# Performance work log

Measured on AMD Instinct MI355X. Metric: run time of the kernel, lower is better.

## Reference

```python
import jax, jax.numpy as jnp
import numpy as np

NEG_SLOPE = 0.2  # PyG GATConv leaky_relu negative_slope
EPS = 1e-16      # PyG softmax denominator epsilon


def _add_self_loops(edge_index, edge_attr, N):
    # PyG add_self_loops with fill_value='mean': loop attr = mean of incoming edge attrs
    src, dst = edge_index[0], edge_index[1]
    ones = jnp.ones((src.shape[0],), edge_attr.dtype)
    cnt = jax.ops.segment_sum(ones, dst, num_segments=N)
    loop_attr = jax.ops.segment_sum(edge_attr, dst, num_segments=N) / jnp.maximum(cnt, 1.0)[:, None]
    loops = jnp.arange(N, dtype=src.dtype)
    return (jnp.concatenate([src, loops]),
            jnp.concatenate([dst, loops]),
            jnp.concatenate([edge_attr, loop_attr], axis=0))


def _gat_conv(x, src, dst, ea, W, We, att_src, att_dst, att_edge, bias, heads, out_ch):
    N = x.shape[0]
    h = (x @ W).reshape(N, heads, out_ch)              # [N,H,C]
    a_src = (h * att_src).sum(-1)                      # [N,H]
    a_dst = (h * att_dst).sum(-1)                      # [N,H]
    e = (ea @ We).reshape(-1, heads, out_ch)           # [E,H,C]
    a_edge = (e * att_edge).sum(-1)                    # [E,H]
    alpha = jax.nn.leaky_relu(a_src[src] + a_dst[dst] + a_edge, NEG_SLOPE)
    amax = jax.ops.segment_max(alpha, dst, num_segments=N)
    alpha = jnp.exp(alpha - amax[dst])
    denom = jax.ops.segment_sum(alpha, dst, num_segments=N)
    alpha = alpha / (denom[dst] + EPS)
    out = jax.ops.segment_sum(h[src] * alpha[..., None], dst, num_segments=N)  # [N,H,C]
    return out.mean(axis=1) + bias                     # concat=False -> mean over heads


def setup_inputs() -> dict:
    key = jax.random.key(0)
    ks = jax.random.split(key, 16)
    N, E, F_in, HID, OUT, H = 50000, 800000, 64, 16, 8, 8
    s = 0.1
    return {
        "x": jax.random.normal(ks[0], (N, F_in), jnp.float32),
        "edge_index": jax.random.randint(ks[1], (2, E), 0, N, dtype=jnp.int64),
        "edge_attr": jax.random.uniform(ks[2], (E, 1), jnp.float32),
        "W1": jax.random.normal(ks[3], (F_in, H * HID), jnp.float32) * s,
        "We1": jax.random.normal(ks[4], (1, H * HID), jnp.float32) * s,
        "att_src1": jax.random.normal(ks[5], (H, HID), jnp.float32) * s,
        "att_dst1": jax.random.normal(ks[6], (H, HID), jnp.float32) * s,
        "att_edge1": jax.random.normal(ks[7], (H, HID), jnp.float32) * s,
        "b1": jnp.zeros((HID,), jnp.float32),
        "W2": jax.random.normal(ks[8], (HID, OUT), jnp.float32) * s,
        "We2": jax.random.normal(ks[9], (1, OUT), jnp.float32) * s,
        "att_src2": jax.random.normal(ks[10], (1, OUT), jnp.float32) * s,
        "att_dst2": jax.random.normal(ks[11], (1, OUT), jnp.float32) * s,
        "att_edge2": jax.random.normal(ks[12], (1, OUT), jnp.float32) * s,
        "b2": jnp.zeros((OUT,), jnp.float32),
    }


def reference(x, edge_index, edge_attr, W1, We1, att_src1, att_dst1, att_edge1, b1,
              W2, We2, att_src2, att_dst2, att_edge2, b2):
    N = x.shape[0]
    src, dst, ea = _add_self_loops(edge_index, edge_attr, N)
    h = jax.nn.relu(_gat_conv(x, src, dst, ea, W1, We1, att_src1, att_dst1, att_edge1, b1, 8, 16))
    # dropout is identity in eval mode
    return _gat_conv(h, src, dst, ea, W2, We2, att_src2, att_dst2, att_edge2, b2, 1, 8)
```

## Files before the change

kernel.cpp:

```cpp
#include <hip/hip_runtime.h>
#include <hip/hip_fp16.h>
#include <math.h>

#define LRELU(x) ((x) > 0.0f ? (x) : 0.2f * (x))
#define EPS 1e-16f

typedef _Float16 half8 __attribute__((ext_vector_type(8)));
typedef float floatx4 __attribute__((ext_vector_type(4)));

#define RNG 4
#define NRR 16384
#define RB  64


__global__ __launch_bounds__(256) void k_hist(int E, int CH, const int* __restrict__ ei,
                                              int* __restrict__ H, int* __restrict__ rank) {
    int r = blockIdx.x / RB, b = blockIdx.x % RB;
    __shared__ int hist[NRR];
    for (int i = threadIdx.x; i < NRR; i += 256) hist[i] = 0;
    __syncthreads();
    int lo = b * CH, hi = min(E, (b + 1) * CH);
    int rlo = r << 14;
#pragma unroll 4
    for (int e = lo + threadIdx.x; e < hi; e += 256) {
        int d = ei[E + e];
        int dr = d - rlo;
        if ((unsigned)dr < NRR) rank[e] = atomicAdd(&hist[dr], 1);
    }
    __syncthreads();
    int* Hb = H + (size_t)blockIdx.x * NRR;
    for (int i = threadIdx.x; i < NRR; i += 256) Hb[i] = hist[i];
}

__global__ __launch_bounds__(256) void k_cntscan(int N, int* __restrict__ H,
                                                 int* rowptr, int* bsums) {
    __shared__ int sm[256];
    int t = threadIdx.x;
    int n = blockIdx.x * 256 + t;
    int sum = 0;
    if (n < N) {
        int r = n >> 14, dr = n & (NRR - 1);
        size_t base = ((size_t)(r * RB)) * NRR + dr;
#pragma unroll 8
        for (int b = 0; b < RB; ++b) {
            size_t idx = base + (size_t)b * NRR;
            int v = H[idx];
            H[idx] = sum;
            sum += v;
        }
    }
    int val = (n < N) ? (sum + 1) : 0;
    sm[t] = val; __syncthreads();
    for (int ofs = 1; ofs < 256; ofs <<= 1) {
        int v = (t >= ofs) ? sm[t - ofs] : 0;
        __syncthreads();
        sm[t] += v;
        __syncthreads();
    }
    if (n < N) rowptr[n] = sm[t] - val;
    if (t == 255) bsums[blockIdx.x] = sm[255];
}

__global__ void k_scan2(int nb, int N, int* bsums, int* rowptr) {
    __shared__ int sm[256];
    int t = threadIdx.x;
    int v = (t < nb) ? bsums[t] : 0;
    sm[t] = v; __syncthreads();
    for (int ofs = 1; ofs < 256; ofs <<= 1) {
        int u = (t >= ofs) ? sm[t - ofs] : 0;
        __syncthreads();
        sm[t] += u;
        __syncthreads();
    }
    if (t < nb) bsums[t] = sm[t] - v;
    if (t == 255) rowptr[N] = sm[255];
}

__global__ void k_scan3(int N, int* rowptr, const int* __restrict__ bsums) {
    int n = blockIdx.x * blockDim.x + threadIdx.x;
    if (n < N) rowptr[n] += bsums[n >> 8];
}

__global__ void k_scatter(int E, int CH, const int* __restrict__ ei, const float* __restrict__ ea,
                          const int* __restrict__ rowptr, const int* __restrict__ H,
                          const int* __restrict__ rank, int2* __restrict__ rec) {
    int e = blockIdx.x * blockDim.x + threadIdx.x;
    if (e >= E) return;
    int s = ei[e], d = ei[E + e];
    int r = d >> 14, dr = d & (NRR - 1);
    int b = e / CH;
    int pos = rowptr[d] + H[((size_t)(r * RB + b)) * NRR + dr] + rank[e];
    unsigned long long pk = ((unsigned long long)(unsigned)__float_as_int(ea[e]) << 32)
                          | (unsigned long long)(unsigned)s;
    __builtin_nontemporal_store(pk, (unsigned long long*)&rec[pos]);
}


__global__ __launch_bounds__(256) void k_misc(
    int N, int nbN, int Mpad, const int* __restrict__ rowptr, int2* __restrict__ rec,
    const float* __restrict__ x, _Float16* __restrict__ xh,
    const float* __restrict__ W1, _Float16* __restrict__ Wpk,
    const float* __restrict__ We1, const float* __restrict__ ae1,
    const float* __restrict__ We2, const float* __restrict__ ae2,
    float* __restrict__ wed) {
    int bid = blockIdx.x;
    if (bid < nbN) {
        int d = bid * 256 + threadIdx.x;
        if (d < N) {
            int start = rowptr[d], slot = rowptr[d + 1] - 1;
            float ssum = 0.0f;
            for (int i = start; i < slot; ++i) ssum += __int_as_float(rec[i].y);
            float mean = ssum / fmaxf((float)(slot - start), 1.0f);
            rec[slot] = make_int2(d, __float_as_int(mean));
        }
    } else if (bid < nbN + Mpad / 32) {
        int t = (bid - nbN) * 256 + threadIdx.x;
        int row = t >> 3;
        half8 h;
        if (row < N) {
            const float4* pp = (const float4*)(x + (size_t)t * 8);
            float4 f0 = pp[0], f1 = pp[1];
            h[0] = (_Float16)f0.x; h[1] = (_Float16)f0.y; h[2] = (_Float16)f0.z; h[3] = (_Float16)f0.w;
            h[4] = (_Float16)f1.x; h[5] = (_Float16)f1.y; h[6] = (_Float16)f1.z; h[7] = (_Float16)f1.w;
        } else {
#pragma unroll
            for (int i = 0; i < 8; ++i) h[i] = (_Float16)0.0f;
        }
        *(half8*)(xh + (size_t)t * 8) = h;
    } else {
        int t = threadIdx.x;
        for (int i = 0; i < 32; ++i) {
            int idx = i * 256 + t;
            int j  = idx & 7;
            int lq = (idx >> 3) & 63;
            int ks = (idx >> 9) & 1;
            int ct = idx >> 10;
            int k   = ks * 32 + (lq >> 4) * 8 + j;
            int col = ct * 16 + (lq & 15);
            Wpk[idx] = (_Float16)W1[k * 128 + col];
        }
        if (t < 8) {
            float ssum = 0.0f;
            for (int cc = 0; cc < 16; ++cc) ssum += We1[t * 16 + cc] * ae1[t * 16 + cc];
            wed[t] = ssum;
        }
        if (t == 8) {
            float ssum = 0.0f;
            for (int cc = 0; cc < 8; ++cc) ssum += We2[cc] * ae2[cc];
            wed[8] = ssum;
        }
    }
}


#define LDSP 132

__global__ __launch_bounds__(256) void k_gemm1m(
    int N, const _Float16* __restrict__ xh, const _Float16* __restrict__ Wpk,
    const float* __restrict__ att_s, const float* __restrict__ att_d,
    __half* __restrict__ h1, float* __restrict__ asrc, float* __restrict__ adst) {
    __shared__ float hs[4 * 16 * LDSP];
    int tid = threadIdx.x;
    int w = tid >> 6, l = tid & 63;
    int row0 = blockIdx.x * 64 + w * 16;
    int arow = row0 + (l & 15);
    half8 a0 = *(const half8*)(xh + (size_t)arow * 64 + (l >> 4) * 8);
    half8 a1 = *(const half8*)(xh + (size_t)arow * 64 + 32 + (l >> 4) * 8);
    float* base = &hs[w * 16 * LDSP];
    int r0 = (l >> 4) * 4;
#pragma unroll
    for (int ct = 0; ct < 8; ++ct) {
        half8 b0 = *(const half8*)(Wpk + ((ct * 2 + 0) * 64 + l) * 8);
        half8 b1 = *(const half8*)(Wpk + ((ct * 2 + 1) * 64 + l) * 8);
        floatx4 acc = {0.f, 0.f, 0.f, 0.f};
        acc = __builtin_amdgcn_mfma_f32_16x16x32_f16(a0, b0, acc, 0, 0, 0);
        acc = __builtin_amdgcn_mfma_f32_16x16x32_f16(a1, b1, acc, 0, 0, 0);
        int col = ct * 16 + (l & 15);
#pragma unroll
        for (int i = 0; i < 4; ++i)
            base[(r0 + i) * LDSP + col] = acc[i];
    }
    __syncthreads();
    int r = tid >> 2, g = tid & 3;
    int rg = blockIdx.x * 64 + r;
    if (rg >= N) return;
    float v[32];
    const float* rp = &hs[r * LDSP + g * 32];
#pragma unroll
    for (int j = 0; j < 8; ++j) {
        floatx4 t4 = *(const floatx4*)(rp + j * 4);
        v[j * 4 + 0] = t4[0]; v[j * 4 + 1] = t4[1];
        v[j * 4 + 2] = t4[2]; v[j * 4 + 3] = t4[3];
    }
    float vs0 = 0.f, vs1 = 0.f, vd0 = 0.f, vd1 = 0.f;
    const float4* as4 = (const float4*)(att_s + g * 32);
    const float4* ad4 = (const float4*)(att_d + g * 32);
#pragma unroll
    for (int j = 0; j < 4; ++j) {
        float4 a4 = as4[j], d4 = ad4[j];
        vs0 += v[j*4+0]*a4.x + v[j*4+1]*a4.y + v[j*4+2]*a4.z + v[j*4+3]*a4.w;
        vd0 += v[j*4+0]*d4.x + v[j*4+1]*d4.y + v[j*4+2]*d4.z + v[j*4+3]*d4.w;
    }
#pragma unroll
    for (int j = 4; j < 8; ++j) {
        float4 a4 = as4[j], d4 = ad4[j];
        vs1 += v[j*4+0]*a4.x + v[j*4+1]*a4.y + v[j*4+2]*a4.z + v[j*4+3]*a4.w;
        vd1 += v[j*4+0]*d4.x + v[j*4+1]*d4.y + v[j*4+2]*d4.z + v[j*4+3]*d4.w;
    }
    union { __half h[32]; float4 f4[4]; } u;
#pragma unroll
    for (int i = 0; i < 32; ++i) u.h[i] = __float2half(v[i]);
    float4* hp = (float4*)(h1 + (size_t)rg * 128 + g * 32);
#pragma unroll
    for (int j = 0; j < 4; ++j) hp[j] = u.f4[j];
    asrc[rg * 8 + g * 2]     = vs0;
    asrc[rg * 8 + g * 2 + 1] = vs1;
    adst[rg * 8 + g * 2]     = vd0;
    adst[rg * 8 + g * 2 + 1] = vd1;
}


__global__ __launch_bounds__(256) void k_agg1(
    int N, const int* __restrict__ rowptr, const int2* __restrict__ rec,
    const float* __restrict__ asrc1, const float* __restrict__ adst1,
    const float* __restrict__ wed,
    const __half* __restrict__ h1, const float* __restrict__ b1,
    const float* __restrict__ W2, const float* __restrict__ as2w, const float* __restrict__ ad2w,
    float* __restrict__ hh2, float* __restrict__ asrc2, float* __restrict__ adst2) {
    int wid = (blockIdx.x * blockDim.x + threadIdx.x) >> 6;
    if (wid >= N) return;
    int l = threadIdx.x & 63;
    int g = l >> 4, q = l & 15, hq = q >> 1;
    int start = rowptr[wid], end = rowptr[wid + 1];
    int len = end - start;
    int G = (len + 3) >> 2;
    int nIt = (G + 1) >> 1;
    int startB = start + (nIt << 2);
    int endA = min(startB, end);
    float adn = adst1[wid * 8 + hq];
    float wdh = wed[hq];

    float acc[8] = {0.f,0.f,0.f,0.f,0.f,0.f,0.f,0.f};
    float denom = 0.0f;
    int eA = start + g, eB = startB + g;
    int last = end - 1;
    int2 rvA = rec[min(eA, last)];
    int2 rvB = rec[min(eB, last)];
    float avA = asrc1[rvA.x * 8 + hq];
    float avB = asrc1[rvB.x * 8 + hq];
    for (int it = 0; it < nIt; ++it) {
        float4 hvA = *(const float4*)(h1 + ((size_t)rvA.x << 7) + q * 8);
        float4 hvB = *(const float4*)(h1 + ((size_t)rvB.x << 7) + q * 8);
        int eAn = eA + 4, eBn = eB + 4;
        int2 rnA = rec[min(eAn, last)];
        int2 rnB = rec[min(eBn, last)];
        float anA = asrc1[rnA.x * 8 + hq];
        float anB = asrc1[rnB.x * 8 + hq];
        float aA = avA + adn + __int_as_float(rvA.y) * wdh;
        aA = LRELU(aA);
        float pA = (eA < endA) ? __expf(aA) : 0.0f;
        float aB = avB + adn + __int_as_float(rvB.y) * wdh;
        aB = LRELU(aB);
        float pB = (eB < end) ? __expf(aB) : 0.0f;
        denom += pA + pB;
        const _Float16* hpA = (const _Float16*)&hvA;
        const _Float16* hpB = (const _Float16*)&hvB;
#pragma unroll
        for (int k = 0; k < 8; ++k)
            acc[k] = fmaf(pA, (float)hpA[k], fmaf(pB, (float)hpB[k], acc[k]));
        rvA = rnA; avA = anA; rvB = rnB; avB = anB;
        eA = eAn; eB = eBn;
    }
#pragma unroll
    for (int k = 0; k < 8; ++k) {
        acc[k] += __shfl_xor(acc[k], 16);
        acc[k] += __shfl_xor(acc[k], 32);
    }
    denom += __shfl_xor(denom, 16);
    denom += __shfl_xor(denom, 32);
    float inv = 1.0f / (denom + EPS);
    float val[8];
#pragma unroll
    for (int k = 0; k < 8; ++k) {
        float v = acc[k] * inv;
        v += __shfl_xor(v, 2);
        v += __shfl_xor(v, 4);
        v += __shfl_xor(v, 8);
        val[k] = v;
    }
    int par = l & 1;
    int c = (l >> 1) & 7;
    float t8[8];
#pragma unroll
    for (int j = 0; j < 8; ++j)
        t8[j] = fmaxf(val[j] * 0.125f + b1[par * 8 + j], 0.0f);
    float partial = 0.0f;
#pragma unroll
    for (int j = 0; j < 8; ++j)
        partial = fmaf(t8[j], W2[(par * 8 + j) * 8 + c], partial);
    float hhc = partial + __shfl_xor(partial, 1);
    float sdot = hhc * as2w[c];
    float ddot = hhc * ad2w[c];
    sdot += __shfl_xor(sdot, 2); sdot += __shfl_xor(sdot, 4); sdot += __shfl_xor(sdot, 8);
    ddot += __shfl_xor(ddot, 2); ddot += __shfl_xor(ddot, 4); ddot += __shfl_xor(ddot, 8);
    if (l < 16 && par == 0) hh2[(size_t)wid * 8 + c] = hhc;
    if (l == 0) { asrc2[wid] = sdot; adst2[wid] = ddot; }
}


__global__ __launch_bounds__(256) void k_agg2(
    int N, const int* __restrict__ rowptr, const int2* __restrict__ rec,
    const float* __restrict__ asrc2, const float* __restrict__ adst2,
    const float* __restrict__ wed,
    const float* __restrict__ hh, const float* __restrict__ b2, float* __restrict__ out) {
    int wid = (blockIdx.x * blockDim.x + threadIdx.x) >> 6;
    if (wid >= N) return;
    int l = threadIdx.x & 63;
    int eo = l >> 3, c = l & 7;
    int start = rowptr[wid], end = rowptr[wid + 1];
    int len = end - start;
    int G = (len + 7) >> 3;
    int nIt = (G + 1) >> 1;
    int startB = start + (nIt << 3);
    int endA = min(startB, end);
    float adn = adst2[wid];
    float w2 = wed[8];

    float acc = 0.0f, denom = 0.0f;
    int eA = start + eo, eB = startB + eo;
    int last = end - 1;
    int2 rvA = rec[min(eA, last)];
    int2 rvB = rec[min(eB, last)];
    float avA = asrc2[rvA.x];
    float avB = asrc2[rvB.x];
    for (int it = 0; it < nIt; ++it) {
        float hvA = hh[(size_t)rvA.x * 8 + c];
        float hvB = hh[(size_t)rvB.x * 8 + c];
        int eAn = eA + 8, eBn = eB + 8;
        int2 rnA = rec[min(eAn, last)];
        int2 rnB = rec[min(eBn, last)];
        float anA = asrc2[rnA.x];
        float anB = asrc2[rnB.x];
        float aA = avA + adn + __int_as_float(rvA.y) * w2;
        aA = LRELU(aA);
        float pA = (eA < endA) ? __expf(aA) : 0.0f;
        float aB = avB + adn + __int_as_float(rvB.y) * w2;
        aB = LRELU(aB);
        float pB = (eB < end) ? __expf(aB) : 0.0f;
        denom += pA + pB;
        acc = fmaf(pA, hvA, fmaf(pB, hvB, acc));
        rvA = rnA; avA = anA; rvB = rnB; avB = anB;
        eA = eAn; eB = eBn;
    }
    acc += __shfl_xor(acc, 8);  acc += __shfl_xor(acc, 16);  acc += __shfl_xor(acc, 32);
    denom += __shfl_xor(denom, 8); denom += __shfl_xor(denom, 16); denom += __shfl_xor(denom, 32);
    if (l < 8) out[(size_t)wid * 8 + l] = acc / (denom + EPS) + b2[l];
}


extern "C" void kernel_launch(void* const* d_in, const int* in_sizes, int n_in,
                              void* d_out, int out_size, void* d_ws, size_t ws_size,
                              hipStream_t stream) {
    const float* x        = (const float*)d_in[0];
    const int*   ei       = (const int*)d_in[1];
    const float* ea       = (const float*)d_in[2];
    const float* W1       = (const float*)d_in[3];
    const float* We1      = (const float*)d_in[4];
    const float* att_src1 = (const float*)d_in[5];
    const float* att_dst1 = (const float*)d_in[6];
    const float* att_edge1= (const float*)d_in[7];
    const float* b1       = (const float*)d_in[8];
    const float* W2       = (const float*)d_in[9];
    const float* We2      = (const float*)d_in[10];
    const float* att_src2 = (const float*)d_in[11];
    const float* att_dst2 = (const float*)d_in[12];
    const float* att_edge2= (const float*)d_in[13];
    const float* b2       = (const float*)d_in[14];
    float* out = (float*)d_out;

    const int N = in_sizes[0] / 64;
    const int E = in_sizes[2];
    const int E2 = E + N;
    const int CH = (E + RB - 1) / RB;
    const int NB64 = (N + 63) / 64;
    const int Mpad = NB64 * 64;

    char* p = (char*)d_ws;
    auto alloc = [&](size_t bytes) { void* r = (void*)p; p += (bytes + 255) & ~(size_t)255; return r; };
    int*   rowptr = (int*)  alloc((size_t)(N + 1) * 4);
    int*   bsums  = (int*)  alloc((size_t)4096 * 4);
    int2*  rec    = (int2*) alloc((size_t)E2 * 8);
    _Float16* Wpk = (_Float16*)alloc((size_t)8192 * 2);
    __half* h1    = (__half*)alloc((size_t)Mpad * 128 * 2);
    float* asrc1  = (float*)alloc((size_t)N * 8 * 4);
    float* adst1  = (float*)alloc((size_t)N * 8 * 4);
    float* hh2    = (float*)alloc((size_t)N * 8 * 4);
    float* asrc2  = (float*)alloc((size_t)N * 4);
    float* adst2  = (float*)alloc((size_t)N * 4);
    float* wed    = (float*)alloc(16 * 4);
    char* pS = p;
    int*   rank  = (int*)pS;
    int*   H     = (int*)(pS + (((size_t)E * 4 + 255) & ~(size_t)255));
    _Float16* xh = (_Float16*)pS;

    const int nbN = (N + 255) / 256;

    hipLaunchKernelGGL(k_hist,    dim3(RNG * RB), dim3(256), 0, stream, E, CH, ei, H, rank);
    hipLaunchKernelGGL(k_cntscan, dim3(nbN), dim3(256), 0, stream, N, H, rowptr, bsums);
    hipLaunchKernelGGL(k_scan2,   dim3(1), dim3(256), 0, stream, nbN, N, bsums, rowptr);
    hipLaunchKernelGGL(k_scan3,   dim3(nbN), dim3(256), 0, stream, N, rowptr, bsums);
    hipLaunchKernelGGL(k_scatter, dim3((E + 255) / 256), dim3(256), 0, stream, E, CH, ei, ea, rowptr, H, rank, rec);
    hipLaunchKernelGGL(k_misc,    dim3(nbN + Mpad / 32 + 1), dim3(256), 0, stream, N, nbN, Mpad, rowptr,
                       rec, x, xh, W1, Wpk, We1, att_edge1, We2, att_edge2, wed);
    hipLaunchKernelGGL(k_gemm1m,  dim3(NB64), dim3(256), 0, stream, N, xh, Wpk, att_src1, att_dst1, h1, asrc1, adst1);
    hipLaunchKernelGGL(k_agg1,    dim3((N + 3) / 4), dim3(256), 0, stream, N, rowptr, rec, asrc1, adst1, wed,
                       h1, b1, W2, att_src2, att_dst2, hh2, asrc2, adst2);
    hipLaunchKernelGGL(k_agg2,    dim3((N + 3) / 4), dim3(256), 0, stream, N, rowptr, rec, asrc2, adst2, wed,
                       hh2, b2, out);
}
```

Before: 151.1 us.

## Remap layer-1 aggregation lanes to edge-by-head and prescale logits by log2e

In the layer-1 aggregation, each lane now takes one edge-slot and one head, loading 16 halfs per edge. Previously lanes split each 128-wide row into quarters across 4 edge groups, with two interleaved edge streams. The head-mean and W2 projection now go through an LDS transpose instead of shuffle chains. Attention logits are prescaled by log2(e) at production so the kernels use exp2f and a fmaxf-based leaky relu. Both aggregation kernels add a two-deep prefetch of edge records, which adds register pressure and LDS use.

```diff
diff --git a/kernel.cpp b/kernel.cpp
--- a/kernel.cpp
+++ b/kernel.cpp
@@ -2,8 +2,8 @@
 #include <hip/hip_fp16.h>
 #include <math.h>
 
-#define LRELU(x) ((x) > 0.0f ? (x) : 0.2f * (x))
 #define EPS 1e-16f
+#define LOG2E 1.44269504088896340736f
 
 typedef _Float16 half8 __attribute__((ext_vector_type(8)));
 typedef float floatx4 __attribute__((ext_vector_type(4)));
@@ -142,12 +142,12 @@
         if (t < 8) {
             float ssum = 0.0f;
             for (int cc = 0; cc < 16; ++cc) ssum += We1[t * 16 + cc] * ae1[t * 16 + cc];
-            wed[t] = ssum;
+            wed[t] = ssum * LOG2E;
         }
         if (t == 8) {
             float ssum = 0.0f;
             for (int cc = 0; cc < 8; ++cc) ssum += We2[cc] * ae2[cc];
-            wed[8] = ssum;
+            wed[8] = ssum * LOG2E;
         }
     }
 }
@@ -213,10 +213,10 @@
     float4* hp = (float4*)(h1 + (size_t)rg * 128 + g * 32);
 #pragma unroll
     for (int j = 0; j < 4; ++j) hp[j] = u.f4[j];
-    asrc[rg * 8 + g * 2]     = vs0;
-    asrc[rg * 8 + g * 2 + 1] = vs1;
-    adst[rg * 8 + g * 2]     = vd0;
-    adst[rg * 8 + g * 2 + 1] = vd1;
+    asrc[rg * 8 + g * 2]     = vs0 * LOG2E;
+    asrc[rg * 8 + g * 2 + 1] = vs1 * LOG2E;
+    adst[rg * 8 + g * 2]     = vd0 * LOG2E;
+    adst[rg * 8 + g * 2 + 1] = vd1 * LOG2E;
 }
 
 
@@ -224,87 +224,77 @@
     int N, const int* __restrict__ rowptr, const int2* __restrict__ rec,
     const float* __restrict__ asrc1, const float* __restrict__ adst1,
     const float* __restrict__ wed,
-    const __half* __restrict__ h1, const float* __restrict__ b1,
+    const __half* __restrict__ h1v, const float* __restrict__ b1,
     const float* __restrict__ W2, const float* __restrict__ as2w, const float* __restrict__ ad2w,
     float* __restrict__ hh2, float* __restrict__ asrc2, float* __restrict__ adst2) {
-    int wid = (blockIdx.x * blockDim.x + threadIdx.x) >> 6;
+    __shared__ float hs[4 * 1040];
+    int tid = threadIdx.x;
+    int wid = (blockIdx.x * blockDim.x + tid) >> 6;
     if (wid >= N) return;
-    int l = threadIdx.x & 63;
-    int g = l >> 4, q = l & 15, hq = q >> 1;
+    int l = tid & 63, w = tid >> 6;
+    int eo = l >> 3, hd = l & 7;
     int start = rowptr[wid], end = rowptr[wid + 1];
+    int last = end - 1;
     int len = end - start;
-    int G = (len + 3) >> 2;
-    int nIt = (G + 1) >> 1;
-    int startB = start + (nIt << 2);
-    int endA = min(startB, end);
-    float adn = adst1[wid * 8 + hq];
-    float wdh = wed[hq];
-
-    float acc[8] = {0.f,0.f,0.f,0.f,0.f,0.f,0.f,0.f};
-    float denom = 0.0f;
-    int eA = start + g, eB = startB + g;
-    int last = end - 1;
-    int2 rvA = rec[min(eA, last)];
-    int2 rvB = rec[min(eB, last)];
-    float avA = asrc1[rvA.x * 8 + hq];
-    float avB = asrc1[rvB.x * 8 + hq];
+    float adn = adst1[wid * 8 + hd];
+    float wdh = wed[hd];
+    const _Float16* h1p = (const _Float16*)h1v;
+
+    float acc[16];
+#pragma unroll
+    for (int k = 0; k < 16; ++k) acc[k] = 0.f;
+    float denom = 0.f;
+    int e = start + eo;
+    int2 rv  = rec[min(e, last)];
+    int2 rn1 = rec[min(e + 8, last)];
+    float av = asrc1[rv.x * 8 + hd];
+    int nIt = (len + 7) >> 3;
     for (int it = 0; it < nIt; ++it) {
-        float4 hvA = *(const float4*)(h1 + ((size_t)rvA.x << 7) + q * 8);
-        float4 hvB = *(const float4*)(h1 + ((size_t)rvB.x << 7) + q * 8);
-        int eAn = eA + 4, eBn = eB + 4;
-        int2 rnA = rec[min(eAn, last)];
-        int2 rnB = rec[min(eBn, last)];
-        float anA = asrc1[rnA.x * 8 + hq];
-        float anB = asrc1[rnB.x * 8 + hq];
-        float aA = avA + adn + __int_as_float(rvA.y) * wdh;
-        aA = LRELU(aA);
-        float pA = (eA < endA) ? __expf(aA) : 0.0f;
-        float aB = avB + adn + __int_as_float(rvB.y) * wdh;
-        aB = LRELU(aB);
-        float pB = (eB < end) ? __expf(aB) : 0.0f;
-        denom += pA + pB;
-        const _Float16* hpA = (const _Float16*)&hvA;
-        const _Float16* hpB = (const _Float16*)&hvB;
-#pragma unroll
-        for (int k = 0; k < 8; ++k)
-            acc[k] = fmaf(pA, (float)hpA[k], fmaf(pB, (float)hpB[k], acc[k]));
-        rvA = rnA; avA = anA; rvB = rnB; avB = anB;
-        eA = eAn; eB = eBn;
-    }
-#pragma unroll
-    for (int k = 0; k < 8; ++k) {
-        acc[k] += __shfl_xor(acc[k], 16);
-        acc[k] += __shfl_xor(acc[k], 32);
-    }
+        const _Float16* hr = h1p + (((size_t)rv.x) << 7) + hd * 16;
+        float4 hv0 = *(const float4*)hr;
+        float4 hv1 = *(const float4*)(hr + 8);
+        int2 rn2 = rec[min(e + 16, last)];
+        float an = asrc1[rn1.x * 8 + hd];
+        float a = av + adn + __int_as_float(rv.y) * wdh;
+        a = fmaxf(a, 0.2f * a);
+        float p = (e < end) ? exp2f(a) : 0.f;
+        denom += p;
+        const _Float16* x0 = (const _Float16*)&hv0;
+        const _Float16* x1 = (const _Float16*)&hv1;
+#pragma unroll
+        for (int k = 0; k < 8; ++k) acc[k]     = fmaf(p, (float)x0[k], acc[k]);
+#pragma unroll
+        for (int k = 0; k < 8; ++k) acc[8 + k] = fmaf(p, (float)x1[k], acc[8 + k]);
+        rv = rn1; rn1 = rn2; av = an; e += 8;
+    }
+    denom += __shfl_xor(denom, 8);
     denom += __shfl_xor(denom, 16);
     denom += __shfl_xor(denom, 32);
-    float inv = 1.0f / (denom + EPS);
-    float val[8];
-#pragma unroll
-    for (int k = 0; k < 8; ++k) {
-        float v = acc[k] * inv;
-        v += __shfl_xor(v, 2);
-        v += __shfl_xor(v, 4);
-        v += __shfl_xor(v, 8);
-        val[k] = v;
-    }
-    int par = l & 1;
-    int c = (l >> 1) & 7;
-    float t8[8];
-#pragma unroll
-    for (int j = 0; j < 8; ++j)
-        t8[j] = fmaxf(val[j] * 0.125f + b1[par * 8 + j], 0.0f);
-    float partial = 0.0f;
-#pragma unroll
-    for (int j = 0; j < 8; ++j)
-        partial = fmaf(t8[j], W2[(par * 8 + j) * 8 + c], partial);
-    float hhc = partial + __shfl_xor(partial, 1);
-    float sdot = hhc * as2w[c];
-    float ddot = hhc * ad2w[c];
-    sdot += __shfl_xor(sdot, 2); sdot += __shfl_xor(sdot, 4); sdot += __shfl_xor(sdot, 8);
-    ddot += __shfl_xor(ddot, 2); ddot += __shfl_xor(ddot, 4); ddot += __shfl_xor(ddot, 8);
-    if (l < 16 && par == 0) hh2[(size_t)wid * 8 + c] = hhc;
-    if (l == 0) { asrc2[wid] = sdot; adst2[wid] = ddot; }
+    float invd = 1.0f / (denom + EPS);
+    float* hw = &hs[w * 1040];
+#pragma unroll
+    for (int k = 0; k < 16; ++k) hw[k * 65 + l] = acc[k] * invd;
+    int c = l & 15, qt = l >> 4;
+    const float* rp = &hw[c * 65 + qt * 16];
+    float v = 0.f;
+#pragma unroll
+    for (int i = 0; i < 16; ++i) v += rp[i];
+    v += __shfl_xor(v, 16);
+    v += __shfl_xor(v, 32);
+    float t = fmaxf(v * 0.125f + b1[c], 0.f);
+    float p0 = t * W2[c * 8 + 2 * qt];
+    float p1 = t * W2[c * 8 + 2 * qt + 1];
+#pragma unroll
+    for (int m = 1; m <= 8; m <<= 1) {
+        p0 += __shfl_xor(p0, m);
+        p1 += __shfl_xor(p1, m);
+    }
+    if (c == 0) *(float2*)&hh2[(size_t)wid * 8 + 2 * qt] = make_float2(p0, p1);
+    float sd = p0 * as2w[2 * qt] + p1 * as2w[2 * qt + 1];
+    float dd = p0 * ad2w[2 * qt] + p1 * ad2w[2 * qt + 1];
+    sd += __shfl_xor(sd, 16); sd += __shfl_xor(sd, 32);
+    dd += __shfl_xor(dd, 16); dd += __shfl_xor(dd, 32);
+    if (l == 0) { asrc2[wid] = sd * LOG2E; adst2[wid] = dd * LOG2E; }
 }
 
 
@@ -329,28 +319,29 @@
     float acc = 0.0f, denom = 0.0f;
     int eA = start + eo, eB = startB + eo;
     int last = end - 1;
-    int2 rvA = rec[min(eA, last)];
-    int2 rvB = rec[min(eB, last)];
+    int2 rvA  = rec[min(eA, last)];
+    int2 rnA1 = rec[min(eA + 8, last)];
+    int2 rvB  = rec[min(eB, last)];
+    int2 rnB1 = rec[min(eB + 8, last)];
     float avA = asrc2[rvA.x];
     float avB = asrc2[rvB.x];
     for (int it = 0; it < nIt; ++it) {
         float hvA = hh[(size_t)rvA.x * 8 + c];
         float hvB = hh[(size_t)rvB.x * 8 + c];
-        int eAn = eA + 8, eBn = eB + 8;
-        int2 rnA = rec[min(eAn, last)];
-        int2 rnB = rec[min(eBn, last)];
-        float anA = asrc2[rnA.x];
-        float anB = asrc2[rnB.x];
+        int2 rnA2 = rec[min(eA + 16, last)];
+        int2 rnB2 = rec[min(eB + 16, last)];
+        float anA = asrc2[rnA1.x];
+        float anB = asrc2[rnB1.x];
         float aA = avA + adn + __int_as_float(rvA.y) * w2;
-        aA = LRELU(aA);
-        float pA = (eA < endA) ? __expf(aA) : 0.0f;
+        aA = fmaxf(aA, 0.2f * aA);
+        float pA = (eA < endA) ? exp2f(aA) : 0.0f;
         float aB = avB + adn + __int_as_float(rvB.y) * w2;
-        aB = LRELU(aB);
-        float pB = (eB < end) ? __expf(aB) : 0.0f;
+        aB = fmaxf(aB, 0.2f * aB);
+        float pB = (eB < end) ? exp2f(aB) : 0.0f;
         denom += pA + pB;
         acc = fmaf(pA, hvA, fmaf(pB, hvB, acc));
-        rvA = rnA; avA = anA; rvB = rnB; avB = anB;
-        eA = eAn; eB = eBn;
+        rvA = rnA1; rnA1 = rnA2; avA = anA; eA += 8;
+        rvB = rnB1; rnB1 = rnB2; avB = anB; eB += 8;
     }
     acc += __shfl_xor(acc, 8);  acc += __shfl_xor(acc, 16);  acc += __shfl_xor(acc, 32);
     denom += __shfl_xor(denom, 8); denom += __shfl_xor(denom, 16); denom += __shfl_xor(denom, 32);
```

Measured after the change: 143.7 us. 1.05x faster.
